# Optimization experiments

Hardware: AMD Instinct MI355X
Metric: run time of the kernel (lower is better)

The kernel has to match this reference:

```python
import jax, jax.numpy as jnp
import numpy as np

EPS = 1e-5


def setup_inputs() -> dict:
    key = jax.random.key(0)
    ks = jax.random.split(key, 5)
    b, c, L = 2, 512, 1024
    x = jax.random.normal(ks[0], (b, c, L), dtype=jnp.float32)
    gamma = jnp.ones((c,), dtype=jnp.float32)
    beta = jnp.zeros((c,), dtype=jnp.float32)
    w_qkv = jax.random.normal(ks[1], (3 * c, c), dtype=jnp.float32) * (1.0 / np.sqrt(c))
    b_qkv = jax.random.normal(ks[2], (3 * c,), dtype=jnp.float32) * 0.02
    # NOTE: original zero-inits proj_out; we use random weights for a
    # non-degenerate correctness baseline (same math, different init values).
    w_proj = jax.random.normal(ks[3], (c, c), dtype=jnp.float32) * (1.0 / np.sqrt(c))
    b_proj = jnp.zeros((c,), dtype=jnp.float32)
    return {"x": x, "gamma": gamma, "beta": beta, "w_qkv": w_qkv,
            "b_qkv": b_qkv, "w_proj": w_proj, "b_proj": b_proj, "num_heads": 8}


def reference(x, gamma, beta, w_qkv, b_qkv, w_proj, b_proj, num_heads):
    b, c, L = x.shape
    nh = int(num_heads)
    hd = c // nh
    # BatchNorm1d, training mode: stats over (batch, length) per channel
    mean = jnp.mean(x, axis=(0, 2), keepdims=True)
    var = jnp.mean((x - mean) ** 2, axis=(0, 2), keepdims=True)  # biased var
    xn = (x - mean) * jax.lax.rsqrt(var + EPS)
    xn = xn * gamma[None, :, None] + beta[None, :, None]
    # 1x1 conv == matmul over channel axis: (b, 3c, L)
    qkv = jnp.einsum('oc,bcl->bol', w_qkv, xn) + b_qkv[None, :, None]
    # Faithful (quirky) layout: (b, 3*nh, hd, L) -> (b, hd, L, 3*nh)
    qkv = qkv.reshape(b, 3 * nh, hd, L).transpose(0, 2, 3, 1)
    q, k, v = jnp.split(qkv, 3, axis=-1)  # each (b, hd, L, nh)
    scale = (3 * nh) ** (-0.5)  # original scales by qkv's last dim before chunk
    # scores: (b, hd, T, T) -- 'heads' axis is hd due to the layout quirk
    w = jax.nn.softmax(jnp.einsum('bhtd,bhfd->bhtf', q * scale, k), axis=-1)
    a = jnp.einsum('bhtf,bhfd->bhtd', w, v)  # (b, hd, L, nh)
    h = a.transpose(0, 3, 1, 2).reshape(b, c, L)
    h = jnp.einsum('oc,bcl->bol', w_proj, h) + b_proj[None, :, None]
    return x + h
```

## Files before the change

### kernel.cpp

```cpp
#include <hip/hip_runtime.h>
#include <hip/hip_bf16.h>
#include <cstddef>
#include <cstdint>

#define B_ 2
#define C_ 512
#define L_ 1024
#define NH_ 8
#define HD_ 64
#define OC_ 1536

typedef short short8 __attribute__((ext_vector_type(8)));
typedef short short4v __attribute__((ext_vector_type(4)));
typedef float f32x4 __attribute__((ext_vector_type(4)));
typedef __fp16 f16x4 __attribute__((ext_vector_type(4)));
typedef __fp16 f16x2 __attribute__((ext_vector_type(2)));

#if defined(__has_builtin)
#if __has_builtin(__builtin_amdgcn_exp2f)
#define FEXP2(x) __builtin_amdgcn_exp2f(x)
#endif
#endif
#ifndef FEXP2
#define FEXP2(x) exp2f(x)
#endif

__device__ inline float bf_bits_to_f32(unsigned short u) {
  union { unsigned u32; float f; } c; c.u32 = ((unsigned)u) << 16; return c.f;
}
__device__ inline short f32_to_bf_bits(float f) {
  union { float f; unsigned u; } c; c.f = f;
  return (short)((c.u + 0x7FFFu + ((c.u >> 16) & 1u)) >> 16);
}

__device__ __forceinline__ void gl2lds16(const short* g, short* l) {
  __builtin_amdgcn_global_load_lds(
      (const __attribute__((address_space(1))) unsigned*)(const void*)g,
      (__attribute__((address_space(3))) unsigned*)(void*)l, 16, 0, 0);
}

__global__ __launch_bounds__(256) void prep_kernel(
    const float* __restrict__ x, const float* __restrict__ gamma,
    const float* __restrict__ beta, const float* __restrict__ w_qkv,
    const float* __restrict__ w_proj,
    float* __restrict__ s_out, float* __restrict__ t_out,
    short* __restrict__ wq16, short* __restrict__ wpp16)
{
  const int bid = blockIdx.x;
  const int tid = threadIdx.x;
  if (bid < 512) {
    const int ch = bid;
    const float4 v0 = *(const float4*)(x + (size_t)ch * L_ + tid * 4);
    const float4 v1 = *(const float4*)(x + (size_t)(C_ + ch) * L_ + tid * 4);
    float s1 = v0.x + v0.y + v0.z + v0.w + v1.x + v1.y + v1.z + v1.w;
    float s2 = v0.x*v0.x + v0.y*v0.y + v0.z*v0.z + v0.w*v0.w
             + v1.x*v1.x + v1.y*v1.y + v1.z*v1.z + v1.w*v1.w;
    #pragma unroll
    for (int off = 32; off > 0; off >>= 1) {
      s1 += __shfl_down(s1, off);
      s2 += __shfl_down(s2, off);
    }
    __shared__ float r1[4], r2[4];
    const int wid = tid >> 6, lane = tid & 63;
    if (lane == 0) { r1[wid] = s1; r2[wid] = s2; }
    __syncthreads();
    if (tid == 0) {
      const float S1 = r1[0] + r1[1] + r1[2] + r1[3];
      const float S2 = r2[0] + r2[1] + r2[2] + r2[3];
      const float invN = 1.f / (float)(B_ * L_);
      const float mean = S1 * invN;
      const float var  = S2 * invN - mean * mean;
      const float rstd = rsqrtf(var + 1e-5f);
      const float sc = gamma[ch] * rstd;
      s_out[ch] = sc;
      t_out[ch] = beta[ch] - mean * sc;
    }
  } else if (bid < 704) {
    const int base = (bid - 512) * 4096 + tid * 16;
    #pragma unroll
    for (int it = 0; it < 2; ++it) {
      const float4 a0 = *(const float4*)(w_qkv + base + it * 8);
      const float4 a1 = *(const float4*)(w_qkv + base + it * 8 + 4);
      short8 v;
      v[0] = f32_to_bf_bits(a0.x); v[1] = f32_to_bf_bits(a0.y);
      v[2] = f32_to_bf_bits(a0.z); v[3] = f32_to_bf_bits(a0.w);
      v[4] = f32_to_bf_bits(a1.x); v[5] = f32_to_bf_bits(a1.y);
      v[6] = f32_to_bf_bits(a1.z); v[7] = f32_to_bf_bits(a1.w);
      *(short8*)(wq16 + base + it * 8) = v;
    }
  } else {
    #pragma unroll
    for (int grp = 0; grp < 4; ++grp) {
      const int idx = (bid - 704) * 4096 + tid * 16 + grp * 4;
      const int o = idx >> 9, cp = idx & 511;
      short4v v;
      #pragma unroll
      for (int j = 0; j < 4; ++j) {
        const int c = ((cp + j) & 7) * 64 + ((cp + j) >> 3);
        v[j] = f32_to_bf_bits(w_proj[(size_t)o * C_ + c]);
      }
      *(short4v*)(wpp16 + (size_t)o * C_ + cp) = v;
    }
  }
}

__global__ __launch_bounds__(256) void xt_kernel(
    const float* __restrict__ x, const float* __restrict__ s,
    const float* __restrict__ t, short* __restrict__ xT)
{
  __shared__ float T[64][65];
  const int t0 = blockIdx.x * 64, c0 = blockIdx.y * 64, b = blockIdx.z;
  const int tid = threadIdx.x;
  const float* xp = x + (size_t)b * C_ * L_;
  #pragma unroll
  for (int it = 0; it < 4; ++it) {
    const int idx = it * 256 + tid;
    const int rr = idx >> 4, c4 = (idx & 15) * 4;
    const float4 v = *(const float4*)(xp + (size_t)(c0 + rr) * L_ + t0 + c4);
    const float sc = s[c0 + rr], tc = t[c0 + rr];
    T[rr][c4 + 0] = fmaf(v.x, sc, tc);
    T[rr][c4 + 1] = fmaf(v.y, sc, tc);
    T[rr][c4 + 2] = fmaf(v.z, sc, tc);
    T[rr][c4 + 3] = fmaf(v.w, sc, tc);
  }
  __syncthreads();
  #pragma unroll
  for (int it = 0; it < 4; ++it) {
    const int idx = it * 256 + tid;
    const int tt_ = idx >> 4, cc4 = (idx & 15) * 4;
    short4v o;
    #pragma unroll
    for (int j = 0; j < 4; ++j) o[j] = f32_to_bf_bits(T[cc4 + j][tt_]);
    *(short4v*)(xT + ((size_t)b * L_ + t0 + tt_) * C_ + c0 + cc4) = o;
  }
}

template <int MR, int NR, bool OUT_BF16>
__global__ __launch_bounds__(256) void gemm_bt16_kernel(
    const short* __restrict__ A, const short* __restrict__ B,
    const float* __restrict__ bias, const float* __restrict__ res,
    void* __restrict__ Cv, int M, int N, int K,
    size_t sB, size_t sC, size_t sR)
{
  constexpr int BM = MR * 32, BN = NR * 32;
  __shared__ short As[BM * 64];
  __shared__ short Bs[BN * 64];
  const int tid = threadIdx.x;
  const int l = tid & 63, w = tid >> 6;
  const int wr = w >> 1, wc = w & 1;
  const int ll = l & 15;
  const int n0 = blockIdx.x * BN, m0 = blockIdx.y * BM, bz = blockIdx.z;
  const short* Bg = B + (size_t)bz * sB;
  f32x4 acc[MR][NR] = {};

  for (int k0 = 0; k0 < K; k0 += 64) {
    #pragma unroll
    for (int it = 0; it < BM / 32; ++it) {
      const int row0 = w * (BM / 4) + it * 8;
      const int row = row0 + (l >> 3), sl = l & 7;
      gl2lds16(A + (size_t)(m0 + row) * K + k0 + ((sl ^ (row & 7)) * 8),
               As + row0 * 64);
    }
    #pragma unroll
    for (int it = 0; it < BN / 32; ++it) {
      const int row0 = w * (BN / 4) + it * 8;
      const int row = row0 + (l >> 3), sl = l & 7;
      gl2lds16(Bg + (size_t)(n0 + row) * K + k0 + ((sl ^ (row & 7)) * 8),
               Bs + row0 * 64);
    }
    __syncthreads();
    #pragma unroll
    for (int kk = 0; kk < 2; ++kk) {
      short8 af[MR], bfg[NR];
      const int sd = kk * 4 + (l >> 4);
      #pragma unroll
      for (int m = 0; m < MR; ++m) {
        const int ra = wr * MR * 16 + m * 16 + ll;
        af[m] = *(const short8*)(As + ra * 64 + (sd ^ (ra & 7)) * 8);
      }
      #pragma unroll
      for (int n = 0; n < NR; ++n) {
        const int rb = wc * NR * 16 + n * 16 + ll;
        bfg[n] = *(const short8*)(Bs + rb * 64 + (sd ^ (rb & 7)) * 8);
      }
      #pragma unroll
      for (int m = 0; m < MR; ++m)
        #pragma unroll
        for (int n = 0; n < NR; ++n)
          acc[m][n] = __builtin_amdgcn_mfma_f32_16x16x32_bf16(
              af[m], bfg[n], acc[m][n], 0, 0, 0);
    }
    __syncthreads();
  }

  const int rg4 = (l >> 4) * 4;
  __hip_bfloat16* Cb = (__hip_bfloat16*)Cv + (size_t)bz * sC;
  float* Cf = (float*)Cv + (size_t)bz * sC;
  const float* Rp = res + (size_t)bz * sR;
  #pragma unroll
  for (int m = 0; m < MR; ++m) {
    #pragma unroll
    for (int reg = 0; reg < 4; ++reg) {
      const int gm = m0 + wr * MR * 16 + m * 16 + rg4 + reg;
      const float bv = bias[gm];
      #pragma unroll
      for (int n = 0; n < NR; ++n) {
        const int gn = n0 + wc * NR * 16 + n * 16 + ll;
        float v = acc[m][n][reg] + bv;
        if (OUT_BF16) {
          Cb[(size_t)gm * N + gn] = __hip_bfloat16_raw{(unsigned short)f32_to_bf_bits(v)};
        } else {
          v += Rp[(size_t)gm * N + gn];
          Cf[(size_t)gm * N + gn] = v;
        }
      }
    }
  }
}

__global__ __launch_bounds__(256, 4) void attn_kernel(
    const __hip_bfloat16* __restrict__ qkv, short* __restrict__ hT)
{
  __shared__ short Klds[1024 * 8];
  __shared__ __fp16 Vlds[9 * 1024];

  const int tq = blockIdx.x, d = blockIdx.y, b = blockIdx.z;
  const int tid = threadIdx.x;
  const int w = tid >> 6, l = tid & 63;
  const int lh = l >> 4, ll = l & 15;
  const int t0 = tq * 128 + w * 32;
  const short* base = (const short*)qkv + (size_t)b * OC_ * L_;
  short* VldsS = (short*)Vlds;

  #pragma unroll
  for (int it = 0; it < 4; ++it) {
    const int f = it * 256 + tid;
    short8 kv;
    #pragma unroll
    for (int g = 0; g < 8; ++g)
      kv[g] = base[(size_t)((8 + g) * HD_ + d) * L_ + f];
    *(short8*)(Klds + f * 8) = kv;
  }
  #pragma unroll
  for (int it = 0; it < 4; ++it) {
    const int i = it * 256 + tid;
    const int g = i >> 7, fs = i & 127;
    const short8 v = *(const short8*)(
        base + (size_t)((16 + g) * HD_ + d) * L_ + fs * 8);
    unsigned u[4];
    #pragma unroll
    for (int e = 0; e < 4; ++e) {
      const f16x2 p = __builtin_amdgcn_cvt_pkrtz(
          bf_bits_to_f32((unsigned short)v[2 * e]),
          bf_bits_to_f32((unsigned short)v[2 * e + 1]));
      u[e] = __builtin_bit_cast(unsigned, p);
    }
    uint4 uu; uu.x = u[0]; uu.y = u[1]; uu.z = u[2]; uu.w = u[3];
    *(uint4*)(VldsS + g * 1024 + ((fs & ~15) + ((fs & 15) ^ g)) * 8) = uu;
  }
  {
    uint2 ones; ones.x = 0x3C003C00u; ones.y = 0x3C003C00u;
    *(uint2*)(VldsS + 8 * 1024 + tid * 4) = ones;
  }

  short8 bQ[2] = {};
  if (l < 16) {
    #pragma unroll
    for (int tt = 0; tt < 2; ++tt) {
      const int t = t0 + tt * 16 + ll;
      short8 qv;
      #pragma unroll
      for (int g = 0; g < 8; ++g) {
        const float v = bf_bits_to_f32(
            (unsigned short)base[(size_t)(g * HD_ + d) * L_ + t]);
        qv[g] = f32_to_bf_bits(v * 0.29448889f);
      }
      bQ[tt] = qv;
    }
  }

  __syncthreads();

  const int vrow = (ll < 9) ? ll : 8;
  f32x4 accO[2] = {};

  for (int c = 0; c < 8; ++c) {
    short8 ak[8];
    #pragma unroll
    for (int ft = 0; ft < 8; ++ft)
      ak[ft] = *(const short8*)(Klds + (size_t)(c * 128 + ft * 16 + ll) * 8);
    f16x4 av[8];
    #pragma unroll
    for (int ft = 0; ft < 8; ++ft) {
      const int s16 = ft * 2 + (lh >> 1);
      av[ft] = *(const f16x4*)(
          Vlds + vrow * 1024 + c * 128 + ((s16 ^ (vrow & 7)) * 8) + (lh & 1) * 4);
    }
    #pragma unroll
    for (int ft = 0; ft < 8; ++ft) {
      #pragma unroll
      for (int tt = 0; tt < 2; ++tt) {
        const f32x4 s = __builtin_amdgcn_mfma_f32_16x16x32_bf16(
            ak[ft], bQ[tt], (f32x4){0.f, 0.f, 0.f, 0.f}, 0, 0, 0);
        const f16x2 p0 = __builtin_amdgcn_cvt_pkrtz(FEXP2(s[0]), FEXP2(s[1]));
        const f16x2 p1 = __builtin_amdgcn_cvt_pkrtz(FEXP2(s[2]), FEXP2(s[3]));
        union { f16x4 v; uint2 u; } bp;
        bp.u.x = __builtin_bit_cast(unsigned, p0);
        bp.u.y = __builtin_bit_cast(unsigned, p1);
        accO[tt] = __builtin_amdgcn_mfma_f32_16x16x16f16(av[ft], bp.v, accO[tt], 0, 0, 0);
      }
    }
  }

  __syncthreads();
  short* Olds = Klds;
  #pragma unroll
  for (int nt = 0; nt < 2; ++nt) {
    const float sum = __shfl(accO[nt][0], 32 + ll);
    const float inv = 1.f / sum;
    if (lh < 2) {
      const int tl = w * 32 + nt * 16 + ll;
      #pragma unroll
      for (int reg = 0; reg < 4; ++reg)
        Olds[tl * 8 + lh * 4 + reg] = f32_to_bf_bits(accO[nt][reg] * inv);
    }
  }
  __syncthreads();
  if (tid < 128) {
    const short8 ov = *(const short8*)(Olds + tid * 8);
    *(short8*)(hT + ((size_t)b * L_ + tq * 128 + tid) * C_ + d * 8) = ov;
  }
}

extern "C" void kernel_launch(void* const* d_in, const int* in_sizes, int n_in,
                              void* d_out, int out_size, void* d_ws, size_t ws_size,
                              hipStream_t stream) {
  (void)in_sizes; (void)n_in; (void)out_size; (void)ws_size;
  const float* x      = (const float*)d_in[0];
  const float* gamma  = (const float*)d_in[1];
  const float* beta   = (const float*)d_in[2];
  const float* w_qkv  = (const float*)d_in[3];
  const float* b_qkv  = (const float*)d_in[4];
  const float* w_proj = (const float*)d_in[5];
  const float* b_proj = (const float*)d_in[6];
  float* out = (float*)d_out;
  char* wsb = (char*)d_ws;

  float* s_buf = (float*)(wsb + 0);
  float* t_buf = (float*)(wsb + 2048);
  short* wq16  = (short*)(wsb + 4096);
  short* wpp16 = (short*)(wsb + 4096 + 1572864);
  short* xT    = (short*)(wsb + 4096 + 2097152);
  short* qkv   = (short*)(wsb + 4096 + 4194304);
  short* hT    = (short*)(wsb + 4096 + 10485760);

  hipLaunchKernelGGL(prep_kernel, dim3(768), dim3(256), 0, stream,
                     x, gamma, beta, w_qkv, w_proj, s_buf, t_buf, wq16, wpp16);
  hipLaunchKernelGGL(xt_kernel, dim3(L_ / 64, C_ / 64, B_), dim3(256), 0, stream,
                     x, s_buf, t_buf, xT);
  hipLaunchKernelGGL((gemm_bt16_kernel<2, 2, true>),
                     dim3(L_ / 64, OC_ / 64, B_), dim3(256), 0, stream,
                     wq16, xT, b_qkv, (const float*)nullptr, (void*)qkv,
                     OC_, L_, C_, (size_t)L_ * C_, (size_t)OC_ * L_, (size_t)0);
  hipLaunchKernelGGL(attn_kernel, dim3(8, HD_, B_), dim3(256), 0, stream,
                     (const __hip_bfloat16*)qkv, hT);
  hipLaunchKernelGGL((gemm_bt16_kernel<1, 2, false>),
                     dim3(L_ / 64, C_ / 32, B_), dim3(256), 0, stream,
                     wpp16, hT, b_proj, x, (void*)out,
                     C_, L_, C_, (size_t)L_ * C_, (size_t)C_ * L_, (size_t)C_ * L_);
}
```

Before: 49.18 us.

## Switch attention QK to fp16 16x16x16 MFMA with padded V layout

```diff
diff --git a/kernel.cpp b/kernel.cpp
--- a/kernel.cpp
+++ b/kernel.cpp
@@ -221,25 +221,31 @@
 __global__ __launch_bounds__(256, 4) void attn_kernel(
     const __hip_bfloat16* __restrict__ qkv, short* __restrict__ hT)
 {
-  __shared__ short Klds[1024 * 8];
-  __shared__ __fp16 Vlds[9 * 1024];
+  __shared__ __fp16 Klds[1024 * 8];
+  __shared__ __fp16 Vlds[9 * 1032];
 
   const int tq = blockIdx.x, d = blockIdx.y, b = blockIdx.z;
   const int tid = threadIdx.x;
   const int w = tid >> 6, l = tid & 63;
-  const int lh = l >> 4, ll = l & 15;
+  const int hi = l >> 4, ll = l & 15;
   const int t0 = tq * 128 + w * 32;
   const short* base = (const short*)qkv + (size_t)b * OC_ * L_;
+  short* KldsS = (short*)Klds;
   short* VldsS = (short*)Vlds;
 
   #pragma unroll
   for (int it = 0; it < 4; ++it) {
     const int f = it * 256 + tid;
-    short8 kv;
-    #pragma unroll
-    for (int g = 0; g < 8; ++g)
-      kv[g] = base[(size_t)((8 + g) * HD_ + d) * L_ + f];
-    *(short8*)(Klds + f * 8) = kv;
+    unsigned u[4];
+    #pragma unroll
+    for (int e = 0; e < 4; ++e) {
+      const f16x2 p = __builtin_amdgcn_cvt_pkrtz(
+          bf_bits_to_f32((unsigned short)base[(size_t)((8 + 2*e)   * HD_ + d) * L_ + f]),
+          bf_bits_to_f32((unsigned short)base[(size_t)((8 + 2*e+1) * HD_ + d) * L_ + f]));
+      u[e] = __builtin_bit_cast(unsigned, p);
+    }
+    uint4 uu; uu.x = u[0]; uu.y = u[1]; uu.z = u[2]; uu.w = u[3];
+    *(uint4*)(KldsS + f * 8) = uu;
   }
   #pragma unroll
   for (int it = 0; it < 4; ++it) {
@@ -256,73 +262,73 @@
       u[e] = __builtin_bit_cast(unsigned, p);
     }
     uint4 uu; uu.x = u[0]; uu.y = u[1]; uu.z = u[2]; uu.w = u[3];
-    *(uint4*)(VldsS + g * 1024 + ((fs & ~15) + ((fs & 15) ^ g)) * 8) = uu;
+    *(uint4*)(VldsS + g * 1032 + fs * 8) = uu;
   }
   {
     uint2 ones; ones.x = 0x3C003C00u; ones.y = 0x3C003C00u;
-    *(uint2*)(VldsS + 8 * 1024 + tid * 4) = ones;
-  }
-
-  short8 bQ[2] = {};
-  if (l < 16) {
+    *(uint2*)(VldsS + 8 * 1032 + tid * 4) = ones;
+  }
+
+  f16x4 bQ[2] = {};
+  if (l < 32) {
+    const int g0 = 4 * hi;
     #pragma unroll
     for (int tt = 0; tt < 2; ++tt) {
       const int t = t0 + tt * 16 + ll;
-      short8 qv;
-      #pragma unroll
-      for (int g = 0; g < 8; ++g) {
-        const float v = bf_bits_to_f32(
-            (unsigned short)base[(size_t)(g * HD_ + d) * L_ + t]);
-        qv[g] = f32_to_bf_bits(v * 0.29448889f);
-      }
-      bQ[tt] = qv;
+      float q[4];
+      #pragma unroll
+      for (int j = 0; j < 4; ++j)
+        q[j] = bf_bits_to_f32(
+                   (unsigned short)base[(size_t)((g0 + j) * HD_ + d) * L_ + t]) *
+               0.29448889f;
+      const f16x2 a = __builtin_amdgcn_cvt_pkrtz(q[0], q[1]);
+      const f16x2 bb = __builtin_amdgcn_cvt_pkrtz(q[2], q[3]);
+      union { f16x4 v; uint2 u; } m;
+      m.u.x = __builtin_bit_cast(unsigned, a);
+      m.u.y = __builtin_bit_cast(unsigned, bb);
+      bQ[tt] = m.v;
     }
   }
 
   __syncthreads();
 
   const int vrow = (ll < 9) ? ll : 8;
+  const f32x4 z4 = {0.f, 0.f, 0.f, 0.f};
   f32x4 accO[2] = {};
-
+  const __fp16* akB = Klds + ll * 8 + 4 * (hi & 1);
+  const __fp16* avB = Vlds + vrow * 1032 + 4 * hi;
+
+  #pragma unroll
   for (int c = 0; c < 8; ++c) {
-    short8 ak[8];
-    #pragma unroll
-    for (int ft = 0; ft < 8; ++ft)
-      ak[ft] = *(const short8*)(Klds + (size_t)(c * 128 + ft * 16 + ll) * 8);
-    f16x4 av[8];
     #pragma unroll
     for (int ft = 0; ft < 8; ++ft) {
-      const int s16 = ft * 2 + (lh >> 1);
-      av[ft] = *(const f16x4*)(
-          Vlds + vrow * 1024 + c * 128 + ((s16 ^ (vrow & 7)) * 8) + (lh & 1) * 4);
-    }
-    #pragma unroll
-    for (int ft = 0; ft < 8; ++ft) {
+      const f16x4 ak = *(const f16x4*)(akB + c * 1024 + ft * 128);
+      const f16x4 av = *(const f16x4*)(avB + c * 128 + ft * 16);
       #pragma unroll
       for (int tt = 0; tt < 2; ++tt) {
-        const f32x4 s = __builtin_amdgcn_mfma_f32_16x16x32_bf16(
-            ak[ft], bQ[tt], (f32x4){0.f, 0.f, 0.f, 0.f}, 0, 0, 0);
+        const f32x4 s = __builtin_amdgcn_mfma_f32_16x16x16f16(
+            ak, bQ[tt], z4, 0, 0, 0);
         const f16x2 p0 = __builtin_amdgcn_cvt_pkrtz(FEXP2(s[0]), FEXP2(s[1]));
         const f16x2 p1 = __builtin_amdgcn_cvt_pkrtz(FEXP2(s[2]), FEXP2(s[3]));
         union { f16x4 v; uint2 u; } bp;
         bp.u.x = __builtin_bit_cast(unsigned, p0);
         bp.u.y = __builtin_bit_cast(unsigned, p1);
-        accO[tt] = __builtin_amdgcn_mfma_f32_16x16x16f16(av[ft], bp.v, accO[tt], 0, 0, 0);
+        accO[tt] = __builtin_amdgcn_mfma_f32_16x16x16f16(av, bp.v, accO[tt], 0, 0, 0);
       }
     }
   }
 
   __syncthreads();
-  short* Olds = Klds;
+  short* Olds = KldsS;
   #pragma unroll
   for (int nt = 0; nt < 2; ++nt) {
     const float sum = __shfl(accO[nt][0], 32 + ll);
     const float inv = 1.f / sum;
-    if (lh < 2) {
+    if (hi < 2) {
       const int tl = w * 32 + nt * 16 + ll;
       #pragma unroll
       for (int reg = 0; reg < 4; ++reg)
-        Olds[tl * 8 + lh * 4 + reg] = f32_to_bf_bits(accO[nt][reg] * inv);
+        Olds[tl * 8 + hi * 4 + reg] = f32_to_bf_bits(accO[nt][reg] * inv);
     }
   }
   __syncthreads();
```

Measured after the change: 48.94 us. About the same (-0.5%).
